# Kernel tuning notes

Measured on AMD Instinct MI355X. Metric: run time of the kernel, lower is better.

The kernel has to match this reference:

```python
import jax, jax.numpy as jnp
import numpy as np

D_MODEL = 1024
H = 16
D_K = D_MODEL // H


def setup_inputs() -> dict:
    key = jax.random.key(0)
    ks = jax.random.split(key, 12)
    B, S = 2, 2048
    q = jax.random.normal(ks[0], (B, S, D_MODEL), dtype=jnp.float32)
    k = jax.random.normal(ks[1], (B, S, D_MODEL), dtype=jnp.float32)
    v = jax.random.normal(ks[2], (B, S, D_MODEL), dtype=jnp.float32)
    mask = jax.random.randint(ks[3], (1, 1, S, S), 0, 2, dtype=jnp.int32)
    sc = 1.0 / np.sqrt(D_MODEL)
    wq = jax.random.uniform(ks[4], (D_MODEL, D_MODEL), jnp.float32, -sc, sc)
    bq = jax.random.uniform(ks[5], (D_MODEL,), jnp.float32, -sc, sc)
    wk = jax.random.uniform(ks[6], (D_MODEL, D_MODEL), jnp.float32, -sc, sc)
    bk = jax.random.uniform(ks[7], (D_MODEL,), jnp.float32, -sc, sc)
    wv = jax.random.uniform(ks[8], (D_MODEL, D_MODEL), jnp.float32, -sc, sc)
    bv = jax.random.uniform(ks[9], (D_MODEL,), jnp.float32, -sc, sc)
    wo = jax.random.uniform(ks[10], (D_MODEL, D_MODEL), jnp.float32, -sc, sc)
    bo = jax.random.uniform(ks[11], (D_MODEL,), jnp.float32, -sc, sc)
    return {"q": q, "k": k, "v": v, "mask": mask,
            "wq": wq, "bq": bq, "wk": wk, "bk": bk,
            "wv": wv, "bv": bv, "wo": wo, "bo": bo}


def reference(q, k, v, mask, wq, bq, wk, bk, wv, bv, wo, bo):
    B, S, _ = q.shape
    # linear projections (torch Linear: x @ W.T + b)
    query = q @ wq.T + bq
    key = k @ wk.T + bk
    value = v @ wv.T + bv
    # [B, S, D] -> [B, H, S, d_k]
    query = query.reshape(B, S, H, D_K).transpose(0, 2, 1, 3)
    key = key.reshape(B, S, H, D_K).transpose(0, 2, 1, 3)
    value = value.reshape(B, S, H, D_K).transpose(0, 2, 1, 3)
    scores = jnp.einsum('bhqd,bhkd->bhqk', query, key) / jnp.sqrt(
        jnp.asarray(D_K, query.dtype))
    # NOTE: source uses `-1 ** 9` which is -1 in Python, not -1e9 (soft mask)
    scores = jnp.where(mask == 0, jnp.asarray(-1.0, scores.dtype), scores)
    attn = jax.nn.softmax(scores, axis=-1)
    # source calls dropout(attn) but discards the result -> no-op
    x = jnp.einsum('bhqk,bhkd->bhqd', attn, value)
    x = x.transpose(0, 2, 1, 3).reshape(B, S, H * D_K)
    return x @ wo.T + bo
```

## Files before the change

### kernel.cpp

```cpp
#include <hip/hip_runtime.h>
#include <hip/hip_bf16.h>

#define D_MODEL 1024
#define NH 16
#define DK 64
#define S_LEN 2048
#define BATCH 2
#define M_ROWS (BATCH * S_LEN)

typedef float    floatx4 __attribute__((ext_vector_type(4)));
typedef _Float16 half8   __attribute__((ext_vector_type(8)));
typedef _Float16 half4v  __attribute__((ext_vector_type(4)));

#define LOG2E 1.4426950408889634f
#define EXPM1 0.36787944117144233f

__device__ __forceinline__ half8 ldh8(const _Float16* p) {
    return __builtin_bit_cast(half8, *(const uint4*)p);
}
__device__ __forceinline__ void gld16(const void* g, void* l) {
    __builtin_amdgcn_global_load_lds(
        (const __attribute__((address_space(1))) void*)g,
        (__attribute__((address_space(3))) void*)l, 16, 0, 0);
}
__device__ __forceinline__ float dpp_swap1(float x) {
    return __builtin_bit_cast(float,
        __builtin_amdgcn_mov_dpp(__builtin_bit_cast(int, x), 0xB1, 0xF, 0xF, false));
}
__device__ __forceinline__ void rawbar() {
    __builtin_amdgcn_sched_barrier(0);
    __builtin_amdgcn_s_barrier();
    __builtin_amdgcn_sched_barrier(0);
}

__global__ __launch_bounds__(256)
void prep(const float* __restrict__ q, const float* __restrict__ k,
          const float* __restrict__ v, const float* __restrict__ wq,
          const float* __restrict__ wk, const float* __restrict__ wv,
          const float* __restrict__ wo, const int* __restrict__ mask,
          _Float16* __restrict__ Ah, _Float16* __restrict__ Wh,
          unsigned long long* __restrict__ mb) {
    const int y = blockIdx.y;
    if (y < 7) {
        if (y >= 3 && blockIdx.x >= 1024) return;
        const float* src = (y == 0) ? q : (y == 1) ? k : (y == 2) ? v :
                           (y == 3) ? wq : (y == 4) ? wk : (y == 5) ? wv : wo;
        _Float16* dst = (y < 3) ? (Ah + (size_t)y * M_ROWS * 1024)
                                : (Wh + (size_t)(y - 3) * 1024 * 1024);
        const size_t idx = ((size_t)blockIdx.x * 256 + threadIdx.x) * 4;
        float4 f = *(const float4*)&src[idx];
        half4v h = {(_Float16)f.x, (_Float16)f.y, (_Float16)f.z, (_Float16)f.w};
        *(half4v*)&dst[idx] = h;
    } else {
        const int wv_ = threadIdx.x >> 6, lane = threadIdx.x & 63;
#pragma unroll
        for (int i = 0; i < 4; i++) {
            const int gw = blockIdx.x * 16 + wv_ * 4 + i;
            const int row = gw >> 5, wid = gw & 31;
            const int mv = mask[(size_t)row * S_LEN + wid * 64 + lane];
            unsigned long long bal = __ballot(mv != 0);
            if (lane == 0) mb[gw] = bal;
        }
    }
}

template <int OUTMODE>
__global__ __launch_bounds__(256)
void gemm_f16(const _Float16* __restrict__ Abase, const _Float16* __restrict__ Wbase,
              const float* __restrict__ b0, const float* __restrict__ b1,
              const float* __restrict__ b2, void* __restrict__ Obase,
              void* __restrict__ Obase2) {
    __shared__ __align__(16) _Float16 SM[16384];
    _Float16* As = SM;
    _Float16* Ws = SM + 8192;
    const int tid = threadIdx.x;
    const int w = tid >> 6, lane = tid & 63;
    const int l15 = lane & 15, q4 = lane >> 4;
    const int z = (OUTMODE == 1) ? blockIdx.z : 0;
    const int m0 = blockIdx.y * 128, n0 = blockIdx.x * 128;
    const int wm = w >> 1, wn = w & 1;

    const _Float16* A = Abase + (size_t)z * M_ROWS * 1024;
    const _Float16* W = Wbase + (size_t)z * 1024 * 1024;
    const float* bias = (OUTMODE == 1) ? ((z == 0) ? b0 : (z == 1) ? b1 : b2) : b0;

    int srow[4], sseg[4];
#pragma unroll
    for (int i = 0; i < 4; i++) {
        const int slot = i * 256 + tid;
        srow[i] = slot >> 3;
        sseg[i] = ((slot & 7) ^ (srow[i] & 7)) * 8;
    }

    int aoff[4][2], woff[4][2];
#pragma unroll
    for (int r = 0; r < 4; r++) {
        const int ar = wm * 64 + r * 16 + l15;
        const int wr = wn * 64 + r * 16 + l15;
#pragma unroll
        for (int kc = 0; kc < 2; kc++) {
            aoff[r][kc] = (ar * 8 + ((kc * 4 + q4) ^ (ar & 7))) * 8;
            woff[r][kc] = (wr * 8 + ((kc * 4 + q4) ^ (wr & 7))) * 8;
        }
    }

    floatx4 acc[4][4];
#pragma unroll
    for (int r = 0; r < 4; r++)
#pragma unroll
        for (int c = 0; c < 4; c++) acc[r][c] = (floatx4){0.f, 0.f, 0.f, 0.f};

#pragma unroll
    for (int i = 0; i < 4; i++) {
        const int lb = (i * 256 + w * 64) * 8;
        gld16(&A[(size_t)(m0 + srow[i]) * 1024 + sseg[i]], &As[lb]);
        gld16(&W[(size_t)(n0 + srow[i]) * 1024 + sseg[i]], &Ws[lb]);
    }

    for (int k0 = 0; k0 < 1024; k0 += 64) {
        __builtin_amdgcn_sched_barrier(0);
        asm volatile("s_waitcnt vmcnt(0)" ::: "memory");
        rawbar();

        half8 af[4][2], wf[4][2];
#pragma unroll
        for (int r = 0; r < 4; r++)
#pragma unroll
            for (int kc = 0; kc < 2; kc++) {
                af[r][kc] = ldh8(&As[aoff[r][kc]]);
                wf[r][kc] = ldh8(&Ws[woff[r][kc]]);
            }
        asm volatile("s_waitcnt lgkmcnt(0)" ::: "memory");
        rawbar();

        if (k0 < 1024 - 64) {
#pragma unroll
            for (int i = 0; i < 4; i++) {
                const int lb = (i * 256 + w * 64) * 8;
                gld16(&A[(size_t)(m0 + srow[i]) * 1024 + (k0 + 64) + sseg[i]], &As[lb]);
                gld16(&W[(size_t)(n0 + srow[i]) * 1024 + (k0 + 64) + sseg[i]], &Ws[lb]);
            }
        }
        __builtin_amdgcn_sched_barrier(0);

#pragma unroll
        for (int kc = 0; kc < 2; kc++)
#pragma unroll
            for (int r = 0; r < 4; r++)
#pragma unroll
                for (int c = 0; c < 4; c++)
                    acc[r][c] = __builtin_amdgcn_mfma_f32_16x16x32_f16(
                        af[r][kc], wf[c][kc], acc[r][c], 0, 0, 0);
    }

    if (OUTMODE == 0) {
#pragma unroll
        for (int r = 0; r < 4; r++)
#pragma unroll
            for (int c = 0; c < 4; c++) {
                const int n = n0 + wn * 64 + c * 16 + l15;
                const int mbase = m0 + wm * 64 + r * 16 + q4 * 4;
#pragma unroll
                for (int reg = 0; reg < 4; reg++)
                    ((float*)Obase)[(size_t)(mbase + reg) * 1024 + n] =
                        acc[r][c][reg] + bias[n];
            }
    } else {
        const int h0 = n0 >> 6;
        const int bB = m0 >> 11;
        if (z == 2) {
#pragma unroll
            for (int r = 0; r < 4; r++)
#pragma unroll
                for (int c = 0; c < 4; c++) {
                    const int nl = wn * 64 + c * 16 + l15;
                    const int ml = wm * 64 + r * 16 + q4 * 4;
                    half4v hv;
#pragma unroll
                    for (int reg = 0; reg < 4; reg++)
                        hv[reg] = (_Float16)(acc[r][c][reg] + bias[n0 + nl]);
                    const int seg = ml >> 3, wi = ml & 7;
                    *(half4v*)&SM[nl * 128 + ((seg ^ (nl & 7)) << 3) + wi] = hv;
                }
            __syncthreads();
#pragma unroll
            for (int it = 0; it < 8; it++) {
                const int chunk = it * 256 + tid;
                const int row = chunk >> 4, seg = chunk & 15;
                half8 v8 = ldh8(&SM[row * 128 + ((seg ^ (row & 7)) << 3)]);
                const int d = row & 63, hh = row >> 6;
                const int s = (m0 & 2047) + seg * 8;
                *(uint4*)&((_Float16*)Obase2)[
                    (((size_t)((bB * 16 + h0 + hh) * 64 + d)) << 11) + s] =
                    __builtin_bit_cast(uint4, v8);
            }
        } else {
            const float sc = (z == 0) ? 0.125f * LOG2E : 1.0f;
#pragma unroll
            for (int r = 0; r < 4; r++)
#pragma unroll
                for (int c = 0; c < 4; c++) {
                    const int nl = wn * 64 + c * 16 + l15;
                    const int seg = nl >> 3, wi = nl & 7;
                    const float bv = bias[n0 + nl];
#pragma unroll
                    for (int reg = 0; reg < 4; reg++) {
                        const int ml = wm * 64 + r * 16 + q4 * 4 + reg;
                        SM[ml * 128 + ((seg ^ (ml & 7)) << 3) + wi] =
                            (_Float16)((acc[r][c][reg] + bv) * sc);
                    }
                }
            __syncthreads();
            _Float16* Oz = (_Float16*)Obase + (size_t)z * M_ROWS * 1024;
#pragma unroll
            for (int it = 0; it < 8; it++) {
                const int chunk = it * 256 + tid;
                const int row = chunk >> 4, seg = chunk & 15;
                half8 v8 = ldh8(&SM[row * 128 + ((seg ^ (row & 7)) << 3)]);
                const int s = (m0 + row) & 2047;
                const int hh = seg >> 3, d = (seg & 7) * 8;
                *(uint4*)&Oz[(((size_t)((bB * 16 + h0 + hh)) * S_LEN + s) << 6) + d] =
                    __builtin_bit_cast(uint4, v8);
            }
        }
    }
}

__global__ __launch_bounds__(512, 4)
void attn_mfma(const _Float16* __restrict__ Qh, const _Float16* __restrict__ Kh,
               const _Float16* __restrict__ Vt, const unsigned long long* __restrict__ mb,
               _Float16* __restrict__ Xh) {
    __shared__ __align__(16) _Float16 Ks[2][64 * 64];
    __shared__ __align__(16) _Float16 Vs[2][64 * 64];
    __shared__ __align__(16) _Float16 Ps[8][32 * 72];

    const int tid = threadIdx.x;
    const int w = tid >> 6, lane = tid & 63;
    const int z = w >> 2, w4 = w & 3;
    const int t255 = tid & 255;
    const int l15 = lane & 15, q4 = lane >> 4;
    const int bh = blockIdx.y, b = bh >> 4, h = bh & 15;
    const int qb = blockIdx.x * 128 + w4 * 32;
    const int kbase = z * 1024;

    const _Float16* Qg = Qh + ((size_t)bh * S_LEN + qb) * DK;
    const _Float16* Kg = Kh + ((size_t)bh * S_LEN + kbase) * DK;
    const _Float16* Vg = Vt + (size_t)bh * DK * S_LEN + kbase;

    half8 Aq[2][2];
#pragma unroll
    for (int qs = 0; qs < 2; qs++)
#pragma unroll
        for (int ch = 0; ch < 2; ch++)
            Aq[qs][ch] = ldh8(&Qg[(qs * 16 + l15) * DK + ch * 32 + q4 * 8]);

    int grow[2], gseg[2];
#pragma unroll
    for (int i = 0; i < 2; i++) {
        const int slot = i * 256 + t255;
        grow[i] = slot >> 3;
        gseg[i] = ((slot & 7) ^ (grow[i] & 7)) * 8;
    }

    int kb[2];
#pragma unroll
    for (int ch = 0; ch < 2; ch++)
        kb[ch] = l15 * 64 + (((ch * 4 + q4) ^ (l15 & 7)) * 8);

    const unsigned long long* mrow_p = mb + (size_t)(qb + q4 * 4) * (S_LEN / 64) + z * 16;

    floatx4 O[2][4];
#pragma unroll
    for (int qs = 0; qs < 2; qs++)
#pragma unroll
        for (int nt = 0; nt < 4; nt++) O[qs][nt] = (floatx4){0.f, 0.f, 0.f, 0.f};
    floatx4 lacc[2];
    lacc[0] = (floatx4){0.f, 0.f, 0.f, 0.f};
    lacc[1] = (floatx4){0.f, 0.f, 0.f, 0.f};

    half8 onesB;
#pragma unroll
    for (int i = 0; i < 8; i++) onesB[i] = (_Float16)1.0f;

    const bool evenlane = ((lane & 1) == 0);

#pragma unroll
    for (int i = 0; i < 2; i++) {
        const int lb = (i * 256 + w4 * 64) * 8;
        gld16(&Kg[(size_t)grow[i] * DK + gseg[i]], &Ks[z][lb]);
    }
#pragma unroll
    for (int i = 0; i < 2; i++) {
        const int lb = (i * 256 + w4 * 64) * 8;
        gld16(&Vg[(size_t)grow[i] * S_LEN + gseg[i]], &Vs[z][lb]);
    }

    for (int j0 = 0; j0 < 1024; j0 += 64) {
        const int jn = (j0 + 64) & 1023;
        const int jw = j0 >> 6;

        __builtin_amdgcn_sched_barrier(0);
        asm volatile("s_waitcnt vmcnt(2)" ::: "memory");
        rawbar();

#pragma unroll
        for (int qs = 0; qs < 2; qs++) {
            unsigned long long mw[4];
#pragma unroll
            for (int jt = 0; jt < 4; jt++) {
                floatx4 c = (floatx4){0.f, 0.f, 0.f, 0.f};
                __builtin_amdgcn_s_setprio(1);
                c = __builtin_amdgcn_mfma_f32_16x16x32_f16(
                    Aq[qs][0], ldh8(&Ks[z][jt * 1024 + kb[0]]), c, 0, 0, 0);
                c = __builtin_amdgcn_mfma_f32_16x16x32_f16(
                    Aq[qs][1], ldh8(&Ks[z][jt * 1024 + kb[1]]), c, 0, 0, 0);
                __builtin_amdgcn_s_setprio(0);
                if (jt == 0) {
#pragma unroll
                    for (int reg = 0; reg < 4; reg++)
                        mw[reg] = mrow_p[qs * 512 + reg * 32 + jw];
                }
#pragma unroll
                for (int reg = 0; reg < 4; reg++) {
                    const unsigned ttw =
                        (unsigned)(mw[reg] >> (jt >= 2 ? 32 : 0)) >> l15;
                    const unsigned sel = ttw & (1u << ((jt & 1) * 16));
                    float p = __builtin_amdgcn_exp2f(c[reg]);
                    p = sel ? p : EXPM1;
                    const float po = dpp_swap1(p);
                    if (evenlane) {
                        *(unsigned*)&Ps[w][(qs * 16 + q4 * 4 + reg) * 72 +
                                           jt * 16 + l15] =
                            __builtin_bit_cast(unsigned,
                                __builtin_amdgcn_cvt_pkrtz(p, po));
                    }
                }
            }
        }

        rawbar();
#pragma unroll
        for (int i = 0; i < 2; i++) {
            const int lb = (i * 256 + w4 * 64) * 8;
            gld16(&Kg[(size_t)(jn + grow[i]) * DK + gseg[i]], &Ks[z][lb]);
        }

        __builtin_amdgcn_sched_barrier(0);
        asm volatile("s_waitcnt vmcnt(2)" ::: "memory");
        rawbar();

#pragma unroll
        for (int qs = 0; qs < 2; qs++) {
            half8 Ap[2];
#pragma unroll
            for (int ch = 0; ch < 2; ch++)
                Ap[ch] = ldh8(&Ps[w][(qs * 16 + l15) * 72 + ch * 32 + q4 * 8]);
            __builtin_amdgcn_s_setprio(1);
            lacc[qs] = __builtin_amdgcn_mfma_f32_16x16x32_f16(Ap[0], onesB, lacc[qs], 0, 0, 0);
            lacc[qs] = __builtin_amdgcn_mfma_f32_16x16x32_f16(Ap[1], onesB, lacc[qs], 0, 0, 0);
#pragma unroll
            for (int nt = 0; nt < 4; nt++) {
                O[qs][nt] = __builtin_amdgcn_mfma_f32_16x16x32_f16(
                    Ap[0], ldh8(&Vs[z][nt * 1024 + kb[0]]), O[qs][nt], 0, 0, 0);
                O[qs][nt] = __builtin_amdgcn_mfma_f32_16x16x32_f16(
                    Ap[1], ldh8(&Vs[z][nt * 1024 + kb[1]]), O[qs][nt], 0, 0, 0);
            }
            __builtin_amdgcn_s_setprio(0);
        }

        rawbar();
#pragma unroll
        for (int i = 0; i < 2; i++) {
            const int lb = (i * 256 + w4 * 64) * 8;
            gld16(&Vg[(size_t)grow[i] * S_LEN + jn + gseg[i]], &Vs[z][lb]);
        }
    }
    __builtin_amdgcn_sched_barrier(0);

    float* Obuf = (float*)&Ps[0][0];
    if (z == 1) {
#pragma unroll
        for (int qs = 0; qs < 2; qs++)
#pragma unroll
            for (int reg = 0; reg < 4; reg++) {
                const int rl = w4 * 32 + qs * 16 + q4 * 4 + reg;
#pragma unroll
                for (int nt = 0; nt < 4; nt++)
                    Obuf[rl * 65 + nt * 16 + l15] = O[qs][nt][reg];
                if (l15 == 0) Obuf[rl * 65 + 64] = lacc[qs][reg];
            }
    }
    __syncthreads();
    if (z == 0) {
#pragma unroll
        for (int qs = 0; qs < 2; qs++)
#pragma unroll
            for (int reg = 0; reg < 4; reg++) {
                const int rl = w4 * 32 + qs * 16 + q4 * 4 + reg;
                const float inv = 1.0f / (lacc[qs][reg] + Obuf[rl * 65 + 64]);
                const int srow = qb + qs * 16 + q4 * 4 + reg;
                _Float16* Xrow = Xh + (size_t)(b * S_LEN + srow) * 1024 + h * DK;
#pragma unroll
                for (int nt = 0; nt < 4; nt++)
                    Xrow[nt * 16 + l15] =
                        (_Float16)((O[qs][nt][reg] + Obuf[rl * 65 + nt * 16 + l15]) * inv);
            }
    }
}

extern "C" void kernel_launch(void* const* d_in, const int* in_sizes, int n_in,
                              void* d_out, int out_size, void* d_ws, size_t ws_size,
                              hipStream_t stream) {
    const float* q  = (const float*)d_in[0];
    const float* k  = (const float*)d_in[1];
    const float* v  = (const float*)d_in[2];
    const int* mask = (const int*)d_in[3];
    const float* wq = (const float*)d_in[4];
    const float* bq = (const float*)d_in[5];
    const float* wk = (const float*)d_in[6];
    const float* bk = (const float*)d_in[7];
    const float* wv = (const float*)d_in[8];
    const float* bv = (const float*)d_in[9];
    const float* wo = (const float*)d_in[10];
    const float* bo = (const float*)d_in[11];
    float* out = (float*)d_out;

    char* ws = (char*)d_ws;
    const size_t MB = 1u << 20;
    _Float16* Wh   = (_Float16*)ws;
    _Float16* Ah   = (_Float16*)(ws + 8 * MB);
    _Float16* QKVh = (_Float16*)(ws + 32 * MB);
    _Float16* Vt   = (_Float16*)(ws + 56 * MB);
    unsigned long long* mb = (unsigned long long*)(ws + 64 * MB);
    _Float16* Xh   = Ah;

    prep<<<dim3(4096, 8), 256, 0, stream>>>(q, k, v, wq, wk, wv, wo, mask,
                                            Ah, Wh, mb);

    gemm_f16<1><<<dim3(8, 32, 3), 256, 0, stream>>>(Ah, Wh, bq, bk, bv, QKVh, Vt);

    attn_mfma<<<dim3(16, 32), 512, 0, stream>>>(QKVh, QKVh + (size_t)M_ROWS * 1024,
                                                Vt, mb, Xh);

    gemm_f16<0><<<dim3(8, 32, 1), 256, 0, stream>>>(Xh, Wh + (size_t)3 * 1024 * 1024,
                                                    bo, bo, bo, out, nullptr);
}
```

Measured before the change: 257.9 us.

## Fuse fp32-to-fp16 conversion into GEMM loads and prefetch attention mask words

Removes the separate prep pass that converted q/k/v and all four weight matrices to fp16 in workspace. The GEMMs now load fp32 tiles into registers, convert them, and write them to LDS before each k-step. This avoids a full extra read/write sweep over the inputs and weights, but doubles the bytes each GEMM tile fetches and adds register pressure plus VALU conversion work inside the main loop. Mask packing becomes its own small kernel. Separately, the attention kernel now loads the packed mask words for the next key block one iteration ahead, so that load latency is hidden behind the MFMA work.

```diff
diff --git a/kernel.cpp b/kernel.cpp
--- a/kernel.cpp
+++ b/kernel.cpp
@@ -23,6 +23,14 @@
         (const __attribute__((address_space(1))) void*)g,
         (__attribute__((address_space(3))) void*)l, 16, 0, 0);
 }
+__device__ __forceinline__ half8 cvt8(float4 a, float4 b) {
+    half8 h;
+    h[0] = (_Float16)a.x; h[1] = (_Float16)a.y;
+    h[2] = (_Float16)a.z; h[3] = (_Float16)a.w;
+    h[4] = (_Float16)b.x; h[5] = (_Float16)b.y;
+    h[6] = (_Float16)b.z; h[7] = (_Float16)b.w;
+    return h;
+}
 __device__ __forceinline__ float dpp_swap1(float x) {
     return __builtin_bit_cast(float,
         __builtin_amdgcn_mov_dpp(__builtin_bit_cast(int, x), 0xB1, 0xF, 0xF, false));
@@ -34,39 +42,24 @@
 }
 
 __global__ __launch_bounds__(256)
-void prep(const float* __restrict__ q, const float* __restrict__ k,
-          const float* __restrict__ v, const float* __restrict__ wq,
-          const float* __restrict__ wk, const float* __restrict__ wv,
-          const float* __restrict__ wo, const int* __restrict__ mask,
-          _Float16* __restrict__ Ah, _Float16* __restrict__ Wh,
-          unsigned long long* __restrict__ mb) {
-    const int y = blockIdx.y;
-    if (y < 7) {
-        if (y >= 3 && blockIdx.x >= 1024) return;
-        const float* src = (y == 0) ? q : (y == 1) ? k : (y == 2) ? v :
-                           (y == 3) ? wq : (y == 4) ? wk : (y == 5) ? wv : wo;
-        _Float16* dst = (y < 3) ? (Ah + (size_t)y * M_ROWS * 1024)
-                                : (Wh + (size_t)(y - 3) * 1024 * 1024);
-        const size_t idx = ((size_t)blockIdx.x * 256 + threadIdx.x) * 4;
-        float4 f = *(const float4*)&src[idx];
-        half4v h = {(_Float16)f.x, (_Float16)f.y, (_Float16)f.z, (_Float16)f.w};
-        *(half4v*)&dst[idx] = h;
-    } else {
-        const int wv_ = threadIdx.x >> 6, lane = threadIdx.x & 63;
-#pragma unroll
-        for (int i = 0; i < 4; i++) {
-            const int gw = blockIdx.x * 16 + wv_ * 4 + i;
-            const int row = gw >> 5, wid = gw & 31;
-            const int mv = mask[(size_t)row * S_LEN + wid * 64 + lane];
-            unsigned long long bal = __ballot(mv != 0);
-            if (lane == 0) mb[gw] = bal;
-        }
+void mask_pack(const int* __restrict__ mask, unsigned long long* __restrict__ mb) {
+    const int wv_ = threadIdx.x >> 6, lane = threadIdx.x & 63;
+#pragma unroll
+    for (int i = 0; i < 4; i++) {
+        const int gw = blockIdx.x * 16 + wv_ * 4 + i;
+        const int row = gw >> 5, wid = gw & 31;
+        const int mv = mask[(size_t)row * S_LEN + wid * 64 + lane];
+        unsigned long long bal = __ballot(mv != 0);
+        if (lane == 0) mb[gw] = bal;
     }
 }
 
 template <int OUTMODE>
 __global__ __launch_bounds__(256)
-void gemm_f16(const _Float16* __restrict__ Abase, const _Float16* __restrict__ Wbase,
+void gemm_f16(const void* __restrict__ Aq_, const void* __restrict__ Ak_,
+              const void* __restrict__ Av_,
+              const float* __restrict__ Wq_, const float* __restrict__ Wk_,
+              const float* __restrict__ Wv_,
               const float* __restrict__ b0, const float* __restrict__ b1,
               const float* __restrict__ b2, void* __restrict__ Obase,
               void* __restrict__ Obase2) {
@@ -80,8 +73,10 @@
     const int m0 = blockIdx.y * 128, n0 = blockIdx.x * 128;
     const int wm = w >> 1, wn = w & 1;
 
-    const _Float16* A = Abase + (size_t)z * M_ROWS * 1024;
-    const _Float16* W = Wbase + (size_t)z * 1024 * 1024;
+    const float* Af = (OUTMODE == 1)
+        ? (const float*)((z == 0) ? Aq_ : (z == 1) ? Ak_ : Av_) : nullptr;
+    const _Float16* Ah = (OUTMODE == 0) ? (const _Float16*)Aq_ : nullptr;
+    const float* Wf = (z == 0) ? Wq_ : (z == 1) ? Wk_ : Wv_;
     const float* bias = (OUTMODE == 1) ? ((z == 0) ? b0 : (z == 1) ? b1 : b2) : b0;
 
     int srow[4], sseg[4];
@@ -110,16 +105,41 @@
 #pragma unroll
         for (int c = 0; c < 4; c++) acc[r][c] = (floatx4){0.f, 0.f, 0.f, 0.f};
 
+    float4 ra[4][2], rw[4][2];
+
+    if (OUTMODE == 1) {
+#pragma unroll
+        for (int i = 0; i < 4; i++) {
+            const float* p = &Af[(size_t)(m0 + srow[i]) * 1024 + sseg[i]];
+            ra[i][0] = *(const float4*)p;
+            ra[i][1] = *(const float4*)(p + 4);
+        }
+    } else {
+#pragma unroll
+        for (int i = 0; i < 4; i++)
+            gld16(&Ah[(size_t)(m0 + srow[i]) * 1024 + sseg[i]],
+                  &As[(i * 256 + w * 64) * 8]);
+    }
 #pragma unroll
     for (int i = 0; i < 4; i++) {
-        const int lb = (i * 256 + w * 64) * 8;
-        gld16(&A[(size_t)(m0 + srow[i]) * 1024 + sseg[i]], &As[lb]);
-        gld16(&W[(size_t)(n0 + srow[i]) * 1024 + sseg[i]], &Ws[lb]);
+        const float* p = &Wf[(size_t)(n0 + srow[i]) * 1024 + sseg[i]];
+        rw[i][0] = *(const float4*)p;
+        rw[i][1] = *(const float4*)(p + 4);
     }
 
     for (int k0 = 0; k0 < 1024; k0 += 64) {
         __builtin_amdgcn_sched_barrier(0);
         asm volatile("s_waitcnt vmcnt(0)" ::: "memory");
+        if (OUTMODE == 1) {
+#pragma unroll
+            for (int i = 0; i < 4; i++)
+                *(uint4*)&As[(size_t)(i * 256 + tid) * 8] =
+                    __builtin_bit_cast(uint4, cvt8(ra[i][0], ra[i][1]));
+        }
+#pragma unroll
+        for (int i = 0; i < 4; i++)
+            *(uint4*)&Ws[(size_t)(i * 256 + tid) * 8] =
+                __builtin_bit_cast(uint4, cvt8(rw[i][0], rw[i][1]));
         rawbar();
 
         half8 af[4][2], wf[4][2];
@@ -134,11 +154,25 @@
         rawbar();
 
         if (k0 < 1024 - 64) {
+            const int kn = k0 + 64;
+            if (OUTMODE == 1) {
+#pragma unroll
+                for (int i = 0; i < 4; i++) {
+                    const float* p = &Af[(size_t)(m0 + srow[i]) * 1024 + kn + sseg[i]];
+                    ra[i][0] = *(const float4*)p;
+                    ra[i][1] = *(const float4*)(p + 4);
+                }
+            } else {
+#pragma unroll
+                for (int i = 0; i < 4; i++)
+                    gld16(&Ah[(size_t)(m0 + srow[i]) * 1024 + kn + sseg[i]],
+                          &As[(i * 256 + w * 64) * 8]);
+            }
 #pragma unroll
             for (int i = 0; i < 4; i++) {
-                const int lb = (i * 256 + w * 64) * 8;
-                gld16(&A[(size_t)(m0 + srow[i]) * 1024 + (k0 + 64) + sseg[i]], &As[lb]);
-                gld16(&W[(size_t)(n0 + srow[i]) * 1024 + (k0 + 64) + sseg[i]], &Ws[lb]);
+                const float* p = &Wf[(size_t)(n0 + srow[i]) * 1024 + kn + sseg[i]];
+                rw[i][0] = *(const float4*)p;
+                rw[i][1] = *(const float4*)(p + 4);
             }
         }
         __builtin_amdgcn_sched_barrier(0);
@@ -284,6 +318,13 @@
 
     const bool evenlane = ((lane & 1) == 0);
 
+    unsigned long long mwc[2][4];
+#pragma unroll
+    for (int qs = 0; qs < 2; qs++)
+#pragma unroll
+        for (int reg = 0; reg < 4; reg++)
+            mwc[qs][reg] = mrow_p[qs * 512 + reg * 32];
+
 #pragma unroll
     for (int i = 0; i < 2; i++) {
         const int lb = (i * 256 + w4 * 64) * 8;
@@ -297,15 +338,21 @@
 
     for (int j0 = 0; j0 < 1024; j0 += 64) {
         const int jn = (j0 + 64) & 1023;
-        const int jw = j0 >> 6;
+        const int jwn = ((j0 >> 6) + 1) & 15;
 
         __builtin_amdgcn_sched_barrier(0);
         asm volatile("s_waitcnt vmcnt(2)" ::: "memory");
         rawbar();
 
+        unsigned long long mwn[2][4];
+#pragma unroll
+        for (int qs = 0; qs < 2; qs++)
+#pragma unroll
+            for (int reg = 0; reg < 4; reg++)
+                mwn[qs][reg] = mrow_p[qs * 512 + reg * 32 + jwn];
+
 #pragma unroll
         for (int qs = 0; qs < 2; qs++) {
-            unsigned long long mw[4];
 #pragma unroll
             for (int jt = 0; jt < 4; jt++) {
                 floatx4 c = (floatx4){0.f, 0.f, 0.f, 0.f};
@@ -315,15 +362,10 @@
                 c = __builtin_amdgcn_mfma_f32_16x16x32_f16(
                     Aq[qs][1], ldh8(&Ks[z][jt * 1024 + kb[1]]), c, 0, 0, 0);
                 __builtin_amdgcn_s_setprio(0);
-                if (jt == 0) {
-#pragma unroll
-                    for (int reg = 0; reg < 4; reg++)
-                        mw[reg] = mrow_p[qs * 512 + reg * 32 + jw];
-                }
 #pragma unroll
                 for (int reg = 0; reg < 4; reg++) {
                     const unsigned ttw =
-                        (unsigned)(mw[reg] >> (jt >= 2 ? 32 : 0)) >> l15;
+                        (unsigned)(mwc[qs][reg] >> (jt >= 2 ? 32 : 0)) >> l15;
                     const unsigned sel = ttw & (1u << ((jt & 1) * 16));
                     float p = __builtin_amdgcn_exp2f(c[reg]);
                     p = sel ? p : EXPM1;
@@ -374,6 +416,12 @@
             const int lb = (i * 256 + w4 * 64) * 8;
             gld16(&Vg[(size_t)grow[i] * S_LEN + jn + gseg[i]], &Vs[z][lb]);
         }
+
+#pragma unroll
+        for (int qs = 0; qs < 2; qs++)
+#pragma unroll
+            for (int reg = 0; reg < 4; reg++)
+                mwc[qs][reg] = mwn[qs][reg];
     }
     __builtin_amdgcn_sched_barrier(0);
 
@@ -427,21 +475,20 @@
 
     char* ws = (char*)d_ws;
     const size_t MB = 1u << 20;
-    _Float16* Wh   = (_Float16*)ws;
-    _Float16* Ah   = (_Float16*)(ws + 8 * MB);
+    _Float16* Xh   = (_Float16*)(ws + 8 * MB);
     _Float16* QKVh = (_Float16*)(ws + 32 * MB);
     _Float16* Vt   = (_Float16*)(ws + 56 * MB);
     unsigned long long* mb = (unsigned long long*)(ws + 64 * MB);
-    _Float16* Xh   = Ah;
-
-    prep<<<dim3(4096, 8), 256, 0, stream>>>(q, k, v, wq, wk, wv, wo, mask,
-                                            Ah, Wh, mb);
-
-    gemm_f16<1><<<dim3(8, 32, 3), 256, 0, stream>>>(Ah, Wh, bq, bk, bv, QKVh, Vt);
+
+    mask_pack<<<4096, 256, 0, stream>>>(mask, mb);
+
+    gemm_f16<1><<<dim3(8, 32, 3), 256, 0, stream>>>(q, k, v, wq, wk, wv,
+                                                    bq, bk, bv, QKVh, Vt);
 
     attn_mfma<<<dim3(16, 32), 512, 0, stream>>>(QKVh, QKVh + (size_t)M_ROWS * 1024,
                                                 Vt, mb, Xh);
 
-    gemm_f16<0><<<dim3(8, 32, 1), 256, 0, stream>>>(Xh, Wh + (size_t)3 * 1024 * 1024,
+    gemm_f16<0><<<dim3(8, 32, 1), 256, 0, stream>>>(Xh, nullptr, nullptr,
+                                                    wo, nullptr, nullptr,
                                                     bo, bo, bo, out, nullptr);
 }
```

After: 291.0 us. 1.13x slower.
